# Optimization experiments

Measured on AMD Instinct MI355X. Metric: run time of the kernel, lower is better.

## Reference

```python
import jax, jax.numpy as jnp
import numpy as np

L = 4096
N_BASES = 4

def setup_inputs() -> dict:
    key = jax.random.key(0)
    ids = jax.random.randint(key, (L,), 0, N_BASES)
    one_hot = jax.nn.one_hot(ids, N_BASES, dtype=jnp.float32)  # [L, 4]
    return {"one_hot": one_hot}

def reference(one_hot) -> jnp.ndarray:
    # out[c, i, j] = one_hot[i, c]          for c < 4
    # out[c, i, j] = one_hot[j, c - 4]      for c >= 4
    Lseq = one_hot.shape[0]
    oh_t = one_hot.T  # [4, L]
    top = jnp.broadcast_to(oh_t[:, :, None], (N_BASES, Lseq, Lseq))  # row one-hot
    bot = jnp.broadcast_to(oh_t[:, None, :], (N_BASES, Lseq, Lseq))  # col one-hot
    return jnp.concatenate([top, bot], axis=0)  # [8, L, L]
```

## Files before the change

kernel.cpp:

```cpp
#include <hip/hip_runtime.h>


constexpr int L  = 4096;
constexpr int NB = 4;

__global__ __launch_bounds__(256) void seq_embed(const float* __restrict__ oh,
                                                 float* __restrict__ out) {
    const int row = blockIdx.x;
    const int c   = row >> 12;
    const int i   = row & (L - 1);
    float4* __restrict__ orow =
        reinterpret_cast<float4*>(out) + (size_t)row * (L / 4);
    const int t = threadIdx.x;

    if (c < NB) {
        const float v = oh[i * NB + c];
        const float4 v4 = make_float4(v, v, v, v);
#pragma unroll
        for (int k = 0; k < 4; ++k)
            orow[t + 256 * k] = v4;
    } else {
        const int cc = c - NB;
#pragma unroll
        for (int k = 0; k < 4; ++k) {
            const int j4 = t + 256 * k;
            const int j  = 4 * j4;
            float4 v;
            v.x = oh[(j + 0) * NB + cc];
            v.y = oh[(j + 1) * NB + cc];
            v.z = oh[(j + 2) * NB + cc];
            v.w = oh[(j + 3) * NB + cc];
            orow[j4] = v;
        }
    }
}

extern "C" void kernel_launch(void* const* d_in, const int* in_sizes, int n_in,
                              void* d_out, int out_size, void* d_ws, size_t ws_size,
                              hipStream_t stream) {
    const float* oh = (const float*)d_in[0];
    float* out = (float*)d_out;
    seq_embed<<<8 * L, 256, 0, stream>>>(oh, out);
}
```

Before: 584.9 us.

## Use persistent grid-stride blocks with LDS-staged one-hot and nontemporal stores

Switches from one block per output row to a fixed grid of 2048 blocks that stride over the whole output. Each block first loads the one-hot matrix into shared memory as a byte-packed transpose, so column rows are read with a single 32-bit LDS load instead of four strided global loads. Output writes use nontemporal stores to avoid polluting the cache with the 512MB write stream. The cost is per-block preload work, 16KB of LDS per block, and per-element index math in the inner loop. Converting the input to bytes assumes it holds only 0 or 1 values.

New measurement: 533.8 us. 8.7% less time.

```diff
diff --git a/kernel.cpp b/kernel.cpp
--- a/kernel.cpp
+++ b/kernel.cpp
@@ -1,44 +1,63 @@
 #include <hip/hip_runtime.h>
 
 
-constexpr int L  = 4096;
-constexpr int NB = 4;
+typedef float f32x4 __attribute__((ext_vector_type(4)));
 
-__global__ __launch_bounds__(256) void seq_embed(const float* __restrict__ oh,
+constexpr int L     = 4096;
+constexpr int NB    = 4;
+constexpr int NBLK  = 2048;
+constexpr int NTHR  = 256;
+constexpr int TOT4  = 8 * L * (L / 4);
+constexpr int STRIDE = NBLK * NTHR;
+constexpr int ITERS  = TOT4 / STRIDE;
+
+__global__ __launch_bounds__(256) void seq_embed(const f32x4* __restrict__ oh4,
                                                  float* __restrict__ out) {
-    const int row = blockIdx.x;
-    const int c   = row >> 12;
-    const int i   = row & (L - 1);
-    float4* __restrict__ orow =
-        reinterpret_cast<float4*>(out) + (size_t)row * (L / 4);
+    __shared__ unsigned char ohT[NB][L];
     const int t = threadIdx.x;
 
-    if (c < NB) {
-        const float v = oh[i * NB + c];
-        const float4 v4 = make_float4(v, v, v, v);
 #pragma unroll
-        for (int k = 0; k < 4; ++k)
-            orow[t + 256 * k] = v4;
-    } else {
-        const int cc = c - NB;
-#pragma unroll
-        for (int k = 0; k < 4; ++k) {
-            const int j4 = t + 256 * k;
-            const int j  = 4 * j4;
-            float4 v;
-            v.x = oh[(j + 0) * NB + cc];
-            v.y = oh[(j + 1) * NB + cc];
-            v.z = oh[(j + 2) * NB + cc];
-            v.w = oh[(j + 3) * NB + cc];
-            orow[j4] = v;
+    for (int k = 0; k < L / NTHR; ++k) {
+        const int p = t + NTHR * k;
+        const f32x4 w = oh4[p];
+        ohT[0][p] = (unsigned char)(w.x != 0.0f);
+        ohT[1][p] = (unsigned char)(w.y != 0.0f);
+        ohT[2][p] = (unsigned char)(w.z != 0.0f);
+        ohT[3][p] = (unsigned char)(w.w != 0.0f);
+    }
+    __syncthreads();
+
+    const float* oh = reinterpret_cast<const float*>(oh4);
+    f32x4* __restrict__ out4 = reinterpret_cast<f32x4*>(out);
+    const int base = blockIdx.x * NTHR + t;
+
+#pragma unroll 8
+    for (int it = 0; it < ITERS; ++it) {
+        const int idx = base + it * STRIDE;
+        const int row = idx >> 10;
+        const int c   = row >> 12;
+        const int i   = row & (L - 1);
+        const int j4  = idx & 1023;
+        f32x4 v;
+        if (c < NB) {
+            const float s = oh[i * NB + c];
+            v = (f32x4){s, s, s, s};
+        } else {
+            const unsigned u =
+                *reinterpret_cast<const unsigned*>(&ohT[c - NB][4 * j4]);
+            v.x = (float)((u)       & 0xff);
+            v.y = (float)((u >> 8)  & 0xff);
+            v.z = (float)((u >> 16) & 0xff);
+            v.w = (float)((u >> 24) & 0xff);
         }
+        __builtin_nontemporal_store(v, &out4[idx]);
     }
 }
 
 extern "C" void kernel_launch(void* const* d_in, const int* in_sizes, int n_in,
                               void* d_out, int out_size, void* d_ws, size_t ws_size,
                               hipStream_t stream) {
-    const float* oh = (const float*)d_in[0];
+    const f32x4* oh4 = (const f32x4*)d_in[0];
     float* out = (float*)d_out;
-    seq_embed<<<8 * L, 256, 0, stream>>>(oh, out);
+    seq_embed<<<NBLK, NTHR, 0, stream>>>(oh4, out);
 }
```
